# Optimization experiments

Measured on AMD Instinct MI355X. Metric: run time of the kernel, lower is better.

## Reference

```python
import jax, jax.numpy as jnp
import numpy as np

H = 1024  # hidden size

def setup_inputs() -> dict:
    key = jax.random.key(0)
    k1, k2, k3, k4 = jax.random.split(key, 4)
    stdv = 1.0 / np.sqrt(H)
    x = jax.random.normal(k1, (64, 512, 512), dtype=jnp.float32)
    U = jax.random.uniform(k2, (512, 4 * H), dtype=jnp.float32, minval=-stdv, maxval=stdv)
    W = jax.random.uniform(k3, (H, 4 * H), dtype=jnp.float32, minval=-stdv, maxval=stdv)
    bias = jax.random.uniform(k4, (4 * H,), dtype=jnp.float32, minval=-stdv, maxval=stdv)
    return {"x": x, "U": U, "W": W, "bias": bias}

def _lstm(x, U, W, bias):
    bs, seq, _ = x.shape
    h0 = jnp.zeros((bs, H), dtype=x.dtype)
    c0 = jnp.zeros((bs, H), dtype=x.dtype)
    # Precompute input projections for all timesteps: [seq, bs, 4H]
    xU = jnp.einsum('bsi,ig->sbg', x, U) + bias

    def step(carry, xu_t):
        h_t, c_t = carry
        gates = xu_t + h_t @ W  # [bs, 4H]
        i_t = jax.nn.sigmoid(gates[:, :H])
        f_t = jax.nn.sigmoid(gates[:, H:2 * H])
        g_t = jnp.tanh(gates[:, 2 * H:3 * H])
        o_t = jax.nn.sigmoid(gates[:, 3 * H:])
        c_new = f_t * c_t + i_t * g_t
        h_new = o_t * jnp.tanh(c_new)
        return (h_new, c_new), h_new

    (h_T, c_T), hs = jax.lax.scan(step, (h0, c0), xU)
    hidden_seq = jnp.transpose(hs, (1, 0, 2))  # [bs, seq, H]
    return hidden_seq, (h_T, c_T)

def reference(x, U, W, bias):
    return _lstm(x, U, W, bias)
```

## Files before the change

### kernel.cpp

```cpp
#include <hip/hip_runtime.h>


typedef _Float16 f16x8 __attribute__((ext_vector_type(8)));
typedef float f32x4 __attribute__((ext_vector_type(4)));

__device__ __forceinline__ unsigned short f2h_bits(float f) {
  union { _Float16 h; unsigned short u; } cv;
  cv.h = (_Float16)f;
  return cv.u;
}
__device__ __forceinline__ unsigned int aload(unsigned int* p) {
  return __hip_atomic_load(p, __ATOMIC_RELAXED, __HIP_MEMORY_SCOPE_AGENT);
}
__device__ __forceinline__ void astore(unsigned int* p, unsigned int v) {
  __hip_atomic_store(p, v, __ATOMIC_RELAXED, __HIP_MEMORY_SCOPE_AGENT);
}
__device__ __forceinline__ unsigned long long aload64(unsigned long long* p) {
  return __hip_atomic_load(p, __ATOMIC_RELAXED, __HIP_MEMORY_SCOPE_AGENT);
}


__global__ void cast_x_kernel(const float* __restrict__ x, unsigned short* __restrict__ xh) {
  int i = blockIdx.x * 256 + threadIdx.x;
  float4 v = ((const float4*)x)[i];
  ushort4 o;
  o.x = f2h_bits(v.x); o.y = f2h_bits(v.y);
  o.z = f2h_bits(v.z); o.w = f2h_bits(v.w);
  ((ushort4*)xh)[i] = o;
}

__global__ void pack_W_kernel(const float* __restrict__ W, unsigned short* __restrict__ Wp) {
  int idx = blockIdx.x * 256 + threadIdx.x;
  int l  = idx & 63;
  int kt = (idx >> 6) & 31;
  int T  = idx >> 11;
  int q = T >> 6, jt = T & 63;
  int g  = q * 1024 + jt * 16 + (l & 15);
  int kb = kt * 32 + ((l >> 4) << 3);
  unsigned short tmp[8];
#pragma unroll
  for (int j = 0; j < 8; ++j) tmp[j] = f2h_bits(W[(size_t)(kb + j) * 4096 + g]);
  ((uint4*)Wp)[idx] = *(const uint4*)tmp;
}

__global__ void pack_U_kernel(const float* __restrict__ U, unsigned short* __restrict__ Up) {
  int idx = blockIdx.x * 256 + threadIdx.x;
  int l  = idx & 63;
  int kt = (idx >> 6) & 15;
  int T  = idx >> 10;
  int q = T >> 6, jt = T & 63;
  int g  = q * 1024 + jt * 16 + (l & 15);
  int kb = kt * 32 + ((l >> 4) << 3);
  unsigned short tmp[8];
#pragma unroll
  for (int j = 0; j < 8; ++j) tmp[j] = f2h_bits(U[(size_t)(kb + j) * 4096 + g]);
  ((uint4*)Up)[idx] = *(const uint4*)tmp;
}


#define OUT_HS 33554432

__global__ __launch_bounds__(256, 1) void lstm_rec_kernel(
    const unsigned short* __restrict__ xh,
    const unsigned short* __restrict__ Wp,
    const unsigned short* __restrict__ Up,
    const float* __restrict__ bias,
    float* __restrict__ out,
    unsigned int* hb,
    unsigned int* flags)
{
  __shared__ unsigned short lx[2][16 * 520];
  __shared__ unsigned short lh[16 * 1032];
  __shared__ float gl[4][16][16];

  const int tid  = threadIdx.x;
  const int lane = tid & 63;
  const int wq   = tid >> 6;
  const int m    = lane & 15;
  const int quad = lane >> 4;

  const int bx  = blockIdx.x;
  const int x8  = bx & 7;
  const int grp = x8 >> 1;
  const int jt  = ((bx >> 3) << 1) | (x8 & 1);
  const int b0  = grp * 16;
  const int T   = wq * 64 + jt;

  f16x8 wf[32];
  {
    const f16x8* src = (const f16x8*)Wp + (size_t)T * 2048 + lane;
#pragma unroll
    for (int kt = 0; kt < 32; ++kt) wf[kt] = src[kt * 64];
  }
  f16x8 uf[16];
  {
    const f16x8* src = (const f16x8*)Up + (size_t)T * 1024 + lane;
#pragma unroll
    for (int k2 = 0; k2 < 16; ++k2) uf[k2] = src[k2 * 64];
  }
  const float bias_v = bias[wq * 1024 + jt * 16 + m];

  const int eb = tid >> 4, ej = tid & 15;
  const int b_out = b0 + eb;
  const int j_out = jt * 16 + ej;
  float c = 0.f;

  unsigned int* my_flag   = flags + grp * 256 + jt * 4 + wq;
  unsigned int* grp_flags = flags + grp * 256;

  const uint2* xsrc = (const uint2*)xh;

  uint2 xr[8];
#pragma unroll
  for (int i = 0; i < 8; ++i) {
    int idx = tid + i * 256, row = idx >> 7, off = idx & 127;
    xr[i] = xsrc[(size_t)((b0 + row) * 512 + 0) * 128 + off];
  }
#pragma unroll
  for (int i = 0; i < 8; ++i) {
    int idx = tid + i * 256, row = idx >> 7, off = idx & 127;
    *(uint2*)&lx[0][row * 520 + off * 4] = xr[i];
  }

  for (int t = 0; t < 512; ++t) {
    __syncthreads();

    if (t < 511) {
#pragma unroll
      for (int i = 0; i < 8; ++i) {
        int idx = tid + i * 256, row = idx >> 7, off = idx & 127;
        xr[i] = xsrc[(size_t)((b0 + row) * 512 + (t + 1)) * 128 + off];
      }
    }

    f32x4 a0 = {bias_v, bias_v, bias_v, bias_v};
    f32x4 a1 = {0.f, 0.f, 0.f, 0.f};

    const unsigned short* lxt = lx[t & 1];
#pragma unroll
    for (int k2 = 0; k2 < 16; ++k2) {
      f16x8 xa = *(const f16x8*)&lxt[m * 520 + k2 * 32 + quad * 8];
      if (k2 & 1) a1 = __builtin_amdgcn_mfma_f32_16x16x32_f16(xa, uf[k2], a1, 0, 0, 0);
      else        a0 = __builtin_amdgcn_mfma_f32_16x16x32_f16(xa, uf[k2], a0, 0, 0, 0);
    }

    if (t > 0) {
      unsigned int* f = grp_flags + lane;
      while (true) {
        unsigned int v0 = aload(f);
        unsigned int v1 = aload(f + 64);
        unsigned int v2 = aload(f + 128);
        unsigned int v3 = aload(f + 192);
        unsigned int mn = v0 < v1 ? v0 : v1;
        unsigned int mn2 = v2 < v3 ? v2 : v3;
        mn = mn < mn2 ? mn : mn2;
        if (!__any((int)(mn < (unsigned int)t))) break;
        __builtin_amdgcn_s_sleep(1);
      }

      unsigned long long* src = (unsigned long long*)hb +
          (size_t)(grp * 2 + ((t - 1) & 1)) * 4096;
      unsigned long long u[16];
#pragma unroll
      for (int i = 0; i < 16; ++i) u[i] = aload64(src + tid + i * 256);
#pragma unroll
      for (int i = 0; i < 16; ++i) {
        int idx = tid + i * 256, row = idx >> 8, off = idx & 255;
        *(unsigned long long*)&lh[row * 1032 + off * 4] = u[i];
      }
      __syncthreads();

#pragma unroll
      for (int kt = 0; kt < 32; ++kt) {
        f16x8 ha = *(const f16x8*)&lh[m * 1032 + kt * 32 + quad * 8];
        if (kt & 1) a1 = __builtin_amdgcn_mfma_f32_16x16x32_f16(ha, wf[kt], a1, 0, 0, 0);
        else        a0 = __builtin_amdgcn_mfma_f32_16x16x32_f16(ha, wf[kt], a0, 0, 0, 0);
      }
    }

    if (t < 511) {
#pragma unroll
      for (int i = 0; i < 8; ++i) {
        int idx = tid + i * 256, row = idx >> 7, off = idx & 127;
        *(uint2*)&lx[(t + 1) & 1][row * 520 + off * 4] = xr[i];
      }
    }

#pragma unroll
    for (int r = 0; r < 4; ++r) gl[wq][quad * 4 + r][m] = a0[r] + a1[r];
    __syncthreads();

    float iv = gl[0][eb][ej], fv = gl[1][eb][ej];
    float gv = gl[2][eb][ej], ov = gl[3][eb][ej];
    float ig = 1.f / (1.f + __expf(-iv));
    float fg = 1.f / (1.f + __expf(-fv));
    float og = 1.f / (1.f + __expf(-ov));
    float e2g = __expf(2.f * gv);
    float gg = 1.f - 2.f / (e2g + 1.f);
    c = fg * c + ig * gg;
    float e2c = __expf(2.f * c);
    float tc = 1.f - 2.f / (e2c + 1.f);
    float h = og * tc;

    out[(size_t)b_out * (512 * 1024) + (size_t)t * 1024 + j_out] = h;
    if (t == 511) {
      out[OUT_HS + b_out * 1024 + j_out] = h;
      out[OUT_HS + 65536 + b_out * 1024 + j_out] = c;
    } else {
      unsigned int hbits = (unsigned int)f2h_bits(h);
      unsigned int nbits = (unsigned int)__shfl_down((int)hbits, 1);
      if ((ej & 1) == 0) {
        unsigned int* dst = hb + (size_t)(grp * 2 + (t & 1)) * 8192 +
                            eb * 512 + jt * 8 + (ej >> 1);
        astore(dst, hbits | (nbits << 16));
      }
      asm volatile("s_waitcnt vmcnt(0)" ::: "memory");
      if (lane == 0) astore(my_flag, (unsigned int)(t + 1));
    }
  }
}


extern "C" void kernel_launch(void* const* d_in, const int* in_sizes, int n_in,
                              void* d_out, int out_size, void* d_ws, size_t ws_size,
                              hipStream_t stream) {
  const float* x    = (const float*)d_in[0];
  const float* U    = (const float*)d_in[1];
  const float* W    = (const float*)d_in[2];
  const float* bias = (const float*)d_in[3];
  float* out = (float*)d_out;

  char* p = (char*)d_ws;
  unsigned short* xh = (unsigned short*)p; p += (size_t)64 * 512 * 512 * 2;
  unsigned short* Wp = (unsigned short*)p; p += (size_t)4096 * 1024 * 2;
  unsigned short* Up = (unsigned short*)p; p += (size_t)4096 * 512 * 2;
  unsigned int*   hb = (unsigned int*)p;   p += (size_t)4 * 2 * 16 * 1024 * 2;
  unsigned int* flags = (unsigned int*)p;

  hipMemsetAsync(flags, 0, 4 * 256 * sizeof(unsigned int), stream);
  cast_x_kernel<<<16384, 256, 0, stream>>>(x, xh);
  pack_W_kernel<<<2048, 256, 0, stream>>>(W, Wp);
  pack_U_kernel<<<1024, 256, 0, stream>>>(U, Up);
  lstm_rec_kernel<<<256, 256, 0, stream>>>(xh, Wp, Up, bias, out, hb, flags);
}
```

Baseline: 1.885 ms.

## Embed step tags in hidden-state words to replace separate flag polling

Each hidden-state exchange word becomes 64 bits, with the fp16 pair in the low half and the timestep tag in the high half. Consumers poll the data itself and re-load only the words whose tag is stale. This removes the separate flag array, the vmcnt wait before the flag store, and the second round-trip to load h after the flags are seen. The h loads are also issued before the input-projection MFMAs so their latency overlaps that compute. In exchange, exchange traffic doubles in size and more registers are held across the loop for the speculative loads.

New measurement: 2.773 ms. +47.1%, slower.

```diff
diff --git a/kernel.cpp b/kernel.cpp
--- a/kernel.cpp
+++ b/kernel.cpp
@@ -9,14 +9,11 @@
   cv.h = (_Float16)f;
   return cv.u;
 }
-__device__ __forceinline__ unsigned int aload(unsigned int* p) {
+__device__ __forceinline__ unsigned long long aload64(const unsigned long long* p) {
   return __hip_atomic_load(p, __ATOMIC_RELAXED, __HIP_MEMORY_SCOPE_AGENT);
 }
-__device__ __forceinline__ void astore(unsigned int* p, unsigned int v) {
+__device__ __forceinline__ void astore64(unsigned long long* p, unsigned long long v) {
   __hip_atomic_store(p, v, __ATOMIC_RELAXED, __HIP_MEMORY_SCOPE_AGENT);
-}
-__device__ __forceinline__ unsigned long long aload64(unsigned long long* p) {
-  return __hip_atomic_load(p, __ATOMIC_RELAXED, __HIP_MEMORY_SCOPE_AGENT);
 }
 
 
@@ -66,8 +63,7 @@
     const unsigned short* __restrict__ Up,
     const float* __restrict__ bias,
     float* __restrict__ out,
-    unsigned int* hb,
-    unsigned int* flags)
+    unsigned long long* hb)
 {
   __shared__ unsigned short lx[2][16 * 520];
   __shared__ unsigned short lh[16 * 1032];
@@ -105,9 +101,6 @@
   const int j_out = jt * 16 + ej;
   float c = 0.f;
 
-  unsigned int* my_flag   = flags + grp * 256 + jt * 4 + wq;
-  unsigned int* grp_flags = flags + grp * 256;
-
   const uint2* xsrc = (const uint2*)xh;
 
   uint2 xr[8];
@@ -122,6 +115,8 @@
     *(uint2*)&lx[0][row * 520 + off * 4] = xr[i];
   }
 
+  unsigned long long va[16], vb[16];
+
   for (int t = 0; t < 512; ++t) {
     __syncthreads();
 
@@ -130,6 +125,16 @@
       for (int i = 0; i < 8; ++i) {
         int idx = tid + i * 256, row = idx >> 7, off = idx & 127;
         xr[i] = xsrc[(size_t)((b0 + row) * 512 + (t + 1)) * 128 + off];
+      }
+    }
+
+    const unsigned long long* hsrc =
+        (const unsigned long long*)hb + (size_t)(grp * 2 + ((t - 1) & 1)) * 8192;
+    if (t > 0) {
+#pragma unroll
+      for (int i = 0; i < 16; ++i) {
+        va[i] = aload64(hsrc + i * 512 + tid * 2);
+        vb[i] = aload64(hsrc + i * 512 + tid * 2 + 1);
       }
     }
 
@@ -145,28 +150,27 @@
     }
 
     if (t > 0) {
-      unsigned int* f = grp_flags + lane;
-      while (true) {
-        unsigned int v0 = aload(f);
-        unsigned int v1 = aload(f + 64);
-        unsigned int v2 = aload(f + 128);
-        unsigned int v3 = aload(f + 192);
-        unsigned int mn = v0 < v1 ? v0 : v1;
-        unsigned int mn2 = v2 < v3 ? v2 : v3;
-        mn = mn < mn2 ? mn : mn2;
-        if (!__any((int)(mn < (unsigned int)t))) break;
-        __builtin_amdgcn_s_sleep(1);
-      }
-
-      unsigned long long* src = (unsigned long long*)hb +
-          (size_t)(grp * 2 + ((t - 1) & 1)) * 4096;
-      unsigned long long u[16];
-#pragma unroll
-      for (int i = 0; i < 16; ++i) u[i] = aload64(src + tid + i * 256);
+      const unsigned int want = (unsigned int)t;
+      for (;;) {
+        bool ok = true;
+#pragma unroll
+        for (int i = 0; i < 16; ++i) {
+          if ((unsigned int)(va[i] >> 32) != want) ok = false;
+          if ((unsigned int)(vb[i] >> 32) != want) ok = false;
+        }
+        if (!__any((int)!ok)) break;
+#pragma unroll
+        for (int i = 0; i < 16; ++i) {
+          if ((unsigned int)(va[i] >> 32) != want) va[i] = aload64(hsrc + i * 512 + tid * 2);
+          if ((unsigned int)(vb[i] >> 32) != want) vb[i] = aload64(hsrc + i * 512 + tid * 2 + 1);
+        }
+      }
+
 #pragma unroll
       for (int i = 0; i < 16; ++i) {
-        int idx = tid + i * 256, row = idx >> 8, off = idx & 255;
-        *(unsigned long long*)&lh[row * 1032 + off * 4] = u[i];
+        unsigned long long w = ((unsigned long long)(unsigned int)vb[i] << 32)
+                             | (unsigned long long)(unsigned int)va[i];
+        *(unsigned long long*)&lh[i * 1032 + tid * 4] = w;
       }
       __syncthreads();
 
@@ -210,12 +214,12 @@
       unsigned int hbits = (unsigned int)f2h_bits(h);
       unsigned int nbits = (unsigned int)__shfl_down((int)hbits, 1);
       if ((ej & 1) == 0) {
-        unsigned int* dst = hb + (size_t)(grp * 2 + (t & 1)) * 8192 +
-                            eb * 512 + jt * 8 + (ej >> 1);
-        astore(dst, hbits | (nbits << 16));
-      }
-      asm volatile("s_waitcnt vmcnt(0)" ::: "memory");
-      if (lane == 0) astore(my_flag, (unsigned int)(t + 1));
+        unsigned long long pk = ((unsigned long long)(unsigned int)(t + 1) << 32)
+                              | (unsigned long long)(hbits | (nbits << 16));
+        unsigned long long* dst = hb + (size_t)(grp * 2 + (t & 1)) * 8192
+                                + eb * 512 + jt * 8 + (ej >> 1);
+        astore64(dst, pk);
+      }
     }
   }
 }
@@ -234,12 +238,11 @@
   unsigned short* xh = (unsigned short*)p; p += (size_t)64 * 512 * 512 * 2;
   unsigned short* Wp = (unsigned short*)p; p += (size_t)4096 * 1024 * 2;
   unsigned short* Up = (unsigned short*)p; p += (size_t)4096 * 512 * 2;
-  unsigned int*   hb = (unsigned int*)p;   p += (size_t)4 * 2 * 16 * 1024 * 2;
-  unsigned int* flags = (unsigned int*)p;
-
-  hipMemsetAsync(flags, 0, 4 * 256 * sizeof(unsigned int), stream);
+  unsigned long long* hb = (unsigned long long*)p;
+
+  hipMemsetAsync(hb, 0, (size_t)4 * 2 * 16 * 512 * 8, stream);
   cast_x_kernel<<<16384, 256, 0, stream>>>(x, xh);
   pack_W_kernel<<<2048, 256, 0, stream>>>(W, Wp);
   pack_U_kernel<<<1024, 256, 0, stream>>>(U, Up);
-  lstm_rec_kernel<<<256, 256, 0, stream>>>(xh, Wp, Up, bias, out, hb, flags);
-}
+  lstm_rec_kernel<<<256, 256, 0, stream>>>(xh, Wp, Up, bias, out, hb);
+}
```

## Aggregate per-wave flags into one per-block flag and delay output stores

Applied to the files above, without the earlier changes.

Each block's four waves now count their arrival with an LDS atomic counter. Only the last wave to arrive publishes a single per-block flag, so consumers poll 64 flags instead of 256. The first flag read is issued early, ahead of the x-projection MFMAs, and the barrier at the top of the loop is removed. The hidden-state output store moves after the flag publish, so the vmcnt wait before signalling covers only the small h exchange write rather than the large output write. The risk is subtler ordering between waves, which now depends on the LDS counter and the remaining barriers.

New measurement: 4.128 ms. +119.0%, slower.

```diff
diff --git a/kernel.cpp b/kernel.cpp
--- a/kernel.cpp
+++ b/kernel.cpp
@@ -72,6 +72,7 @@
   __shared__ unsigned short lx[2][16 * 520];
   __shared__ unsigned short lh[16 * 1032];
   __shared__ float gl[4][16][16];
+  __shared__ unsigned int arrive_cnt;
 
   const int tid  = threadIdx.x;
   const int lane = tid & 63;
@@ -105,8 +106,8 @@
   const int j_out = jt * 16 + ej;
   float c = 0.f;
 
-  unsigned int* my_flag   = flags + grp * 256 + jt * 4 + wq;
-  unsigned int* grp_flags = flags + grp * 256;
+  unsigned int* my_flag = flags + grp * 64 + jt;
+  unsigned int* pollp   = flags + grp * 64 + lane;
 
   const uint2* xsrc = (const uint2*)xh;
 
@@ -121,9 +122,12 @@
     int idx = tid + i * 256, row = idx >> 7, off = idx & 127;
     *(uint2*)&lx[0][row * 520 + off * 4] = xr[i];
   }
+  if (tid == 0) arrive_cnt = 0;
+  __syncthreads();
 
   for (int t = 0; t < 512; ++t) {
-    __syncthreads();
+    unsigned int fv = 0;
+    if (t > 0) fv = aload(pollp);
 
     if (t < 511) {
 #pragma unroll
@@ -145,17 +149,9 @@
     }
 
     if (t > 0) {
-      unsigned int* f = grp_flags + lane;
-      while (true) {
-        unsigned int v0 = aload(f);
-        unsigned int v1 = aload(f + 64);
-        unsigned int v2 = aload(f + 128);
-        unsigned int v3 = aload(f + 192);
-        unsigned int mn = v0 < v1 ? v0 : v1;
-        unsigned int mn2 = v2 < v3 ? v2 : v3;
-        mn = mn < mn2 ? mn : mn2;
-        if (!__any((int)(mn < (unsigned int)t))) break;
+      while (__any((int)(fv < (unsigned int)t))) {
         __builtin_amdgcn_s_sleep(1);
+        fv = aload(pollp);
       }
 
       unsigned long long* src = (unsigned long long*)hb +
@@ -190,10 +186,10 @@
     for (int r = 0; r < 4; ++r) gl[wq][quad * 4 + r][m] = a0[r] + a1[r];
     __syncthreads();
 
-    float iv = gl[0][eb][ej], fv = gl[1][eb][ej];
+    float iv = gl[0][eb][ej], fv2 = gl[1][eb][ej];
     float gv = gl[2][eb][ej], ov = gl[3][eb][ej];
     float ig = 1.f / (1.f + __expf(-iv));
-    float fg = 1.f / (1.f + __expf(-fv));
+    float fg = 1.f / (1.f + __expf(-fv2));
     float og = 1.f / (1.f + __expf(-ov));
     float e2g = __expf(2.f * gv);
     float gg = 1.f - 2.f / (e2g + 1.f);
@@ -202,8 +198,8 @@
     float tc = 1.f - 2.f / (e2c + 1.f);
     float h = og * tc;
 
-    out[(size_t)b_out * (512 * 1024) + (size_t)t * 1024 + j_out] = h;
     if (t == 511) {
+      out[(size_t)b_out * (512 * 1024) + (size_t)t * 1024 + j_out] = h;
       out[OUT_HS + b_out * 1024 + j_out] = h;
       out[OUT_HS + 65536 + b_out * 1024 + j_out] = c;
     } else {
@@ -215,7 +211,12 @@
         astore(dst, hbits | (nbits << 16));
       }
       asm volatile("s_waitcnt vmcnt(0)" ::: "memory");
-      if (lane == 0) astore(my_flag, (unsigned int)(t + 1));
+      if (lane == 0) {
+        unsigned int old = atomicAdd(&arrive_cnt, 1u);
+        if (old == 4u * (unsigned int)t + 3u)
+          astore(my_flag, (unsigned int)(t + 1));
+      }
+      out[(size_t)b_out * (512 * 1024) + (size_t)t * 1024 + j_out] = h;
     }
   }
 }
@@ -237,7 +238,7 @@
   unsigned int*   hb = (unsigned int*)p;   p += (size_t)4 * 2 * 16 * 1024 * 2;
   unsigned int* flags = (unsigned int*)p;
 
-  hipMemsetAsync(flags, 0, 4 * 256 * sizeof(unsigned int), stream);
+  hipMemsetAsync(flags, 0, 4 * 64 * sizeof(unsigned int), stream);
   cast_x_kernel<<<16384, 256, 0, stream>>>(x, xh);
   pack_W_kernel<<<2048, 256, 0, stream>>>(W, Wp);
   pack_U_kernel<<<1024, 256, 0, stream>>>(U, Up);
```

## Prefetch flags early, split h load into halves, and defer output store past flag

Applied to the files above, without the earlier changes.

The flag values are now loaded at the start of each timestep so their latency overlaps the input-projection MFMAs, and the spin loop only runs if the first poll shows the step is not ready. The h-state load from global memory is split into two halves, so the first half of the recurrent MFMAs can start while the second half is still being staged into LDS. This adds an extra barrier per step. The full-sequence output store is moved after the flag publish, so the vmcnt wait no longer waits on that large store, which shortens the critical path between timesteps. The top-of-loop barrier is removed, and ordering now relies on the barriers inside the loop.

New measurement: 4.153 ms. 120% more time.

```diff
diff --git a/kernel.cpp b/kernel.cpp
--- a/kernel.cpp
+++ b/kernel.cpp
@@ -121,9 +121,17 @@
     int idx = tid + i * 256, row = idx >> 7, off = idx & 127;
     *(uint2*)&lx[0][row * 520 + off * 4] = xr[i];
   }
+  __syncthreads();
 
   for (int t = 0; t < 512; ++t) {
-    __syncthreads();
+    unsigned int pv0 = 0, pv1 = 0, pv2 = 0, pv3 = 0;
+    unsigned int* fp = grp_flags + lane;
+    if (t > 0) {
+      pv0 = aload(fp);
+      pv1 = aload(fp + 64);
+      pv2 = aload(fp + 128);
+      pv3 = aload(fp + 192);
+    }
 
     if (t < 511) {
 #pragma unroll
@@ -145,33 +153,61 @@
     }
 
     if (t > 0) {
-      unsigned int* f = grp_flags + lane;
-      while (true) {
-        unsigned int v0 = aload(f);
-        unsigned int v1 = aload(f + 64);
-        unsigned int v2 = aload(f + 128);
-        unsigned int v3 = aload(f + 192);
-        unsigned int mn = v0 < v1 ? v0 : v1;
-        unsigned int mn2 = v2 < v3 ? v2 : v3;
+      {
+        unsigned int mn = pv0 < pv1 ? pv0 : pv1;
+        unsigned int mn2 = pv2 < pv3 ? pv2 : pv3;
         mn = mn < mn2 ? mn : mn2;
-        if (!__any((int)(mn < (unsigned int)t))) break;
-        __builtin_amdgcn_s_sleep(1);
+        if (__any((int)(mn < (unsigned int)t))) {
+          while (true) {
+            __builtin_amdgcn_s_sleep(1);
+            unsigned int v0 = aload(fp);
+            unsigned int v1 = aload(fp + 64);
+            unsigned int v2 = aload(fp + 128);
+            unsigned int v3 = aload(fp + 192);
+            unsigned int mna = v0 < v1 ? v0 : v1;
+            unsigned int mnb = v2 < v3 ? v2 : v3;
+            mna = mna < mnb ? mna : mnb;
+            if (!__any((int)(mna < (unsigned int)t))) break;
+          }
+        }
       }
 
       unsigned long long* src = (unsigned long long*)hb +
           (size_t)(grp * 2 + ((t - 1) & 1)) * 4096;
       unsigned long long u[16];
 #pragma unroll
-      for (int i = 0; i < 16; ++i) u[i] = aload64(src + tid + i * 256);
-#pragma unroll
-      for (int i = 0; i < 16; ++i) {
-        int idx = tid + i * 256, row = idx >> 8, off = idx & 255;
-        *(unsigned long long*)&lh[row * 1032 + off * 4] = u[i];
+      for (int i = 0; i < 8; ++i) {
+        int idx = tid + i * 256, row = idx >> 7, colu = idx & 127;
+        u[i] = aload64(src + row * 256 + colu);
+      }
+#pragma unroll
+      for (int i = 0; i < 8; ++i) {
+        int idx = tid + i * 256, row = idx >> 7, colu = idx & 127;
+        u[8 + i] = aload64(src + row * 256 + 128 + colu);
+      }
+#pragma unroll
+      for (int i = 0; i < 8; ++i) {
+        int idx = tid + i * 256, row = idx >> 7, colu = idx & 127;
+        *(unsigned long long*)&lh[row * 1032 + colu * 4] = u[i];
       }
       __syncthreads();
 
 #pragma unroll
-      for (int kt = 0; kt < 32; ++kt) {
+      for (int kt = 0; kt < 16; ++kt) {
+        f16x8 ha = *(const f16x8*)&lh[m * 1032 + kt * 32 + quad * 8];
+        if (kt & 1) a1 = __builtin_amdgcn_mfma_f32_16x16x32_f16(ha, wf[kt], a1, 0, 0, 0);
+        else        a0 = __builtin_amdgcn_mfma_f32_16x16x32_f16(ha, wf[kt], a0, 0, 0, 0);
+      }
+
+#pragma unroll
+      for (int i = 0; i < 8; ++i) {
+        int idx = tid + i * 256, row = idx >> 7, colu = idx & 127;
+        *(unsigned long long*)&lh[row * 1032 + 512 + colu * 4] = u[8 + i];
+      }
+      __syncthreads();
+
+#pragma unroll
+      for (int kt = 16; kt < 32; ++kt) {
         f16x8 ha = *(const f16x8*)&lh[m * 1032 + kt * 32 + quad * 8];
         if (kt & 1) a1 = __builtin_amdgcn_mfma_f32_16x16x32_f16(ha, wf[kt], a1, 0, 0, 0);
         else        a0 = __builtin_amdgcn_mfma_f32_16x16x32_f16(ha, wf[kt], a0, 0, 0, 0);
@@ -202,8 +238,8 @@
     float tc = 1.f - 2.f / (e2c + 1.f);
     float h = og * tc;
 
-    out[(size_t)b_out * (512 * 1024) + (size_t)t * 1024 + j_out] = h;
     if (t == 511) {
+      out[(size_t)b_out * (512 * 1024) + (size_t)t * 1024 + j_out] = h;
       out[OUT_HS + b_out * 1024 + j_out] = h;
       out[OUT_HS + 65536 + b_out * 1024 + j_out] = c;
     } else {
@@ -216,6 +252,7 @@
       }
       asm volatile("s_waitcnt vmcnt(0)" ::: "memory");
       if (lane == 0) astore(my_flag, (unsigned int)(t + 1));
+      out[(size_t)b_out * (512 * 1024) + (size_t)t * 1024 + j_out] = h;
     }
   }
 }
```
